# Kernel tuning notes

Measured on AMD Instinct MI355X. Metric: run time of the kernel, lower is better.

Reference implementation:

```python
import jax, jax.numpy as jnp
import numpy as np

N_DRUG, N_TARGET, N_EDGES, H = 50000, 20000, 500000, 256


def setup_inputs() -> dict:
    key = jax.random.key(0)
    ks = jax.random.split(key, 6)
    s = 1.0 / np.sqrt(2 * H)
    return {
        "z_drug": jax.random.normal(ks[0], (N_DRUG, H), dtype=jnp.float32),
        "z_target": jax.random.normal(ks[1], (N_TARGET, H), dtype=jnp.float32),
        "row": jax.random.randint(ks[2], (N_EDGES,), 0, N_DRUG, dtype=jnp.int64),
        "col": jax.random.randint(ks[3], (N_EDGES,), 0, N_TARGET, dtype=jnp.int64),
        "W1": jax.random.normal(ks[4], (2 * H, H), dtype=jnp.float32) * s,
        "b1": jnp.zeros((H,), dtype=jnp.float32),
        "W2": jax.random.normal(ks[5], (H, 1), dtype=jnp.float32) * (1.0 / np.sqrt(H)),
        "b2": jnp.zeros((1,), dtype=jnp.float32),
    }


def reference(z_drug, z_target, row, col, W1, b1, W2, b2):
    # gather endpoint embeddings by edge index, concat -> [E, 2H]
    zc = jnp.concatenate([z_drug[row], z_target[col]], axis=-1)
    h = jax.nn.relu(zc @ W1 + b1)          # [E, H]
    return h @ W2 + b2                     # [E, 1]
```

## Files before the change

kernel.cpp:

```cpp
#include <hip/hip_runtime.h>
#include <hip/hip_bf16.h>
#include <stdint.h>


typedef unsigned short u16;
typedef __attribute__((ext_vector_type(8))) short short8;
typedef __attribute__((ext_vector_type(4))) float f32x4;

#define HDIM 256
#define KDIM 512
#define BM 128
#define BK 64
#define NWAVE 4

__device__ __forceinline__ u16 f2bf(float f) {
  union { float f; uint32_t u; } v; v.f = f;
  uint32_t u = v.u;
  return (u16)((u + 0x7fffu + ((u >> 16) & 1u)) >> 16);
}

__device__ __forceinline__ void gl2lds16(const void* g, void* l) {
  __builtin_amdgcn_global_load_lds(
      (const __attribute__((address_space(1))) unsigned int*)g,
      (__attribute__((address_space(3))) unsigned int*)l,
      16, 0, 0);
}

#define CVT_BLOCKS 4096
__global__ void prep_kernel(const float* __restrict__ zd_f,
                            const float* __restrict__ zt_f,
                            const float* __restrict__ w1,
                            u16* __restrict__ zdb, u16* __restrict__ ztb,
                            u16* __restrict__ w1t, int n4d, int n4t) {
  const int b = blockIdx.x;
  if (b < 32) {
    __shared__ float tile[64][65];
    const int k0 = (b >> 2) * 64, n0 = (b & 3) * 64;
    const int tx = threadIdx.x & 63, ty = threadIdx.x >> 6;
#pragma unroll
    for (int i = ty; i < 64; i += 4)
      tile[i][tx] = w1[(size_t)(k0 + i) * HDIM + n0 + tx];
    __syncthreads();
#pragma unroll
    for (int i = ty; i < 64; i += 4)
      w1t[(size_t)(n0 + i) * KDIM + k0 + tx] = f2bf(tile[tx][i]);
  } else {
    const int idx = (b - 32) * 256 + threadIdx.x;
    const int stride = CVT_BLOCKS * 256;
    for (int i = idx; i < n4d; i += stride) {
      float4 v = ((const float4*)zd_f)[i];
      ushort4 o; o.x = f2bf(v.x); o.y = f2bf(v.y); o.z = f2bf(v.z); o.w = f2bf(v.w);
      ((ushort4*)zdb)[i] = o;
    }
    for (int i = idx; i < n4t; i += stride) {
      float4 v = ((const float4*)zt_f)[i];
      ushort4 o; o.x = f2bf(v.x); o.y = f2bf(v.y); o.z = f2bf(v.z); o.w = f2bf(v.w);
      ((ushort4*)ztb)[i] = o;
    }
  }
}

__global__ __launch_bounds__(256, 2) void edge_mlp_kernel(
    const u16* __restrict__ zd, const u16* __restrict__ zt,
    const int* __restrict__ row, const int* __restrict__ col,
    const u16* __restrict__ w1t, const float* __restrict__ b1,
    const float* __restrict__ w2, const float* __restrict__ b2,
    float* __restrict__ out, int E) {
  __shared__ u16 lA[BM * BK];
  __shared__ u16 lB[HDIM * BK];
  __shared__ float lP[NWAVE * BM];

  const int tid  = threadIdx.x;
  const int wid  = tid >> 6;
  const int lane = tid & 63;
  const int e0   = blockIdx.x * BM;
  const int r8   = lane >> 3;
  const int slog = ((lane & 7) ^ (r8 & 7)) * 8;

  uint32_t offD[4], offT[4];
#pragma unroll
  for (int t = 0; t < 4; ++t) {
    int ge = min(e0 + wid * 32 + r8 + 8 * t, E - 1);
    offD[t] = (uint32_t)row[ge] * HDIM;
    offT[t] = (uint32_t)col[ge] * HDIM;
  }
  const u16* pB = w1t + (uint32_t)(wid * 64 + r8) * KDIM + slog;

  u16* lAw = &lA[(wid * 32) * BK];
  u16* lBw = &lB[(wid * 64) * BK];

  f32x4 acc[8][4];
#pragma unroll
  for (int i = 0; i < 8; ++i)
#pragma unroll
    for (int j = 0; j < 4; ++j) acc[i][j] = f32x4{0.f, 0.f, 0.f, 0.f};

  const int colid = lane & 15;
  const int quad  = lane >> 4;
  const int csw   = colid & 7;

  for (int kc = 0; kc < 8; ++kc) {
    const int koff = (kc & 3) * BK;
    const u16* zbase = (kc < 4) ? zd : zt;

    __syncthreads();
#pragma unroll
    for (int t = 0; t < 4; ++t) {
      uint32_t o = (kc < 4) ? offD[t] : offT[t];
      gl2lds16(zbase + o + koff + slog, lAw + (8 * t) * BK);
    }
#pragma unroll
    for (int j = 0; j < 8; ++j)
      gl2lds16(pB + (size_t)j * 8 * KDIM + kc * BK, lBw + j * 8 * BK);
    __syncthreads();

#pragma unroll
    for (int ks = 0; ks < BK; ks += 32) {
      const int sl = (ks >> 3) + quad;
      short8 aF[8], bF[4];
#pragma unroll
      for (int rt = 0; rt < 8; ++rt)
        aF[rt] = *(const short8*)&lA[(rt * 16 + colid) * BK + ((sl ^ csw) * 8)];
#pragma unroll
      for (int ct = 0; ct < 4; ++ct)
        bF[ct] = *(const short8*)&lB[(wid * 64 + ct * 16 + colid) * BK + ((sl ^ csw) * 8)];
#pragma unroll
      for (int rt = 0; rt < 8; ++rt)
#pragma unroll
        for (int ct = 0; ct < 4; ++ct)
          acc[rt][ct] = __builtin_amdgcn_mfma_f32_16x16x32_bf16(
              aF[rt], bF[ct], acc[rt][ct], 0, 0, 0);
    }
  }

  float b1v[4], w2v[4];
#pragma unroll
  for (int ct = 0; ct < 4; ++ct) {
    int n = wid * 64 + ct * 16 + colid;
    b1v[ct] = b1[n];
    w2v[ct] = w2[n];
  }
#pragma unroll
  for (int rt = 0; rt < 8; ++rt)
#pragma unroll
    for (int j = 0; j < 4; ++j) {
      float s = 0.f;
#pragma unroll
      for (int ct = 0; ct < 4; ++ct)
        s += fmaxf(acc[rt][ct][j] + b1v[ct], 0.f) * w2v[ct];
#pragma unroll
      for (int off = 8; off >= 1; off >>= 1)
        s += __shfl_xor(s, off, 16);
      if (colid == 0)
        lP[wid * BM + rt * 16 + quad * 4 + j] = s;
    }
  __syncthreads();
  if (tid < BM) {
    int ge = e0 + tid;
    if (ge < E)
      out[ge] = lP[tid] + lP[BM + tid] + lP[2 * BM + tid] + lP[3 * BM + tid]
                + b2[0];
  }
}

__global__ void fallback_kernel(
    const float* __restrict__ zd, const float* __restrict__ zt,
    const int* __restrict__ row, const int* __restrict__ col,
    const float* __restrict__ W1, const float* __restrict__ b1,
    const float* __restrict__ W2, const float* __restrict__ b2,
    float* __restrict__ out, int E) {
  __shared__ float zc[16][512];
  __shared__ float red[4][16];
  const int e0 = blockIdx.x * 16;
  const int tid = threadIdx.x;
  for (int i = tid; i < 16 * 512; i += 256) {
    int e = i >> 9, k = i & 511;
    int ge = min(e0 + e, E - 1);
    zc[e][k] = (k < HDIM) ? zd[(size_t)row[ge] * HDIM + k]
                          : zt[(size_t)col[ge] * HDIM + (k - HDIM)];
  }
  __syncthreads();
  float acc[16];
#pragma unroll
  for (int e = 0; e < 16; ++e) acc[e] = 0.f;
  for (int k = 0; k < KDIM; ++k) {
    float w = W1[k * HDIM + tid];
#pragma unroll
    for (int e = 0; e < 16; ++e) acc[e] += zc[e][k] * w;
  }
  float wv = W2[tid], bv = b1[tid];
  const int lane = tid & 63, wid = tid >> 6;
#pragma unroll
  for (int e = 0; e < 16; ++e) {
    float pv = fmaxf(acc[e] + bv, 0.f) * wv;
#pragma unroll
    for (int off = 32; off >= 1; off >>= 1) pv += __shfl_down(pv, off, 64);
    if (lane == 0) red[wid][e] = pv;
  }
  __syncthreads();
  if (tid < 16) {
    int ge = e0 + tid;
    if (ge < E)
      out[ge] = red[0][tid] + red[1][tid] + red[2][tid] + red[3][tid] + b2[0];
  }
}

extern "C" void kernel_launch(void* const* d_in, const int* in_sizes, int n_in,
                              void* d_out, int out_size, void* d_ws, size_t ws_size,
                              hipStream_t stream) {
  const float* zd_f = (const float*)d_in[0];
  const float* zt_f = (const float*)d_in[1];
  const int*   row  = (const int*)d_in[2];
  const int*   col  = (const int*)d_in[3];
  const float* W1   = (const float*)d_in[4];
  const float* b1   = (const float*)d_in[5];
  const float* W2   = (const float*)d_in[6];
  const float* b2   = (const float*)d_in[7];
  float* out = (float*)d_out;

  const int E  = in_sizes[2];
  const int ND = in_sizes[0] / HDIM;
  const int NT = in_sizes[1] / HDIM;

  size_t off_w1t = 0;
  size_t off_zd  = (size_t)KDIM * HDIM * sizeof(u16);
  size_t off_zt  = off_zd + (size_t)ND * HDIM * sizeof(u16);
  size_t need    = off_zt + (size_t)NT * HDIM * sizeof(u16);

  if (ws_size >= need) {
    u16* w1t = (u16*)((char*)d_ws + off_w1t);
    u16* zdb = (u16*)((char*)d_ws + off_zd);
    u16* ztb = (u16*)((char*)d_ws + off_zt);
    int n4d = ND * HDIM / 4, n4t = NT * HDIM / 4;
    prep_kernel<<<32 + CVT_BLOCKS, 256, 0, stream>>>(zd_f, zt_f, W1,
                                                     zdb, ztb, w1t, n4d, n4t);
    edge_mlp_kernel<<<(E + BM - 1) / BM, 256, 0, stream>>>(
        zdb, ztb, row, col, w1t, b1, W2, b2, out, E);
  } else {
    fallback_kernel<<<(E + 15) / 16, 256, 0, stream>>>(
        zd_f, zt_f, row, col, W1, b1, W2, b2, out, E);
  }
}
```

Measured before the change: 280.8 us.

## Double-buffer LDS tiles and enlarge edge block to 256 with 8 waves

The edge MLP kernel now processes 256 edges per block with 512 threads arranged as a 2x4 wave grid. A and B tiles are double-buffered in LDS so the next K-chunk's global-to-LDS loads are issued while MFMAs run on the current chunk, with one barrier per iteration instead of two. The MFMA sequences are wrapped in s_setprio to favour matrix issue. This halves W1 reloads per edge and hides load latency, at the cost of doubling LDS use (about 96KB per block), which may limit occupancy to one block per CU despite the launch bound.

```diff
diff --git a/kernel.cpp b/kernel.cpp
--- a/kernel.cpp
+++ b/kernel.cpp
@@ -9,9 +9,8 @@
 
 #define HDIM 256
 #define KDIM 512
-#define BM 128
+#define BM 256
 #define BK 64
-#define NWAVE 4
 
 __device__ __forceinline__ u16 f2bf(float f) {
   union { float f; uint32_t u; } v; v.f = f;
@@ -60,15 +59,15 @@
   }
 }
 
-__global__ __launch_bounds__(256, 2) void edge_mlp_kernel(
+__global__ __launch_bounds__(512, 2) void edge_mlp_kernel(
     const u16* __restrict__ zd, const u16* __restrict__ zt,
     const int* __restrict__ row, const int* __restrict__ col,
     const u16* __restrict__ w1t, const float* __restrict__ b1,
     const float* __restrict__ w2, const float* __restrict__ b2,
     float* __restrict__ out, int E) {
-  __shared__ u16 lA[BM * BK];
-  __shared__ u16 lB[HDIM * BK];
-  __shared__ float lP[NWAVE * BM];
+  __shared__ u16 lA[2][BM * BK];
+  __shared__ u16 lB[2][HDIM * BK];
+  __shared__ float lP[4 * BM];
 
   const int tid  = threadIdx.x;
   const int wid  = tid >> 6;
@@ -76,6 +75,8 @@
   const int e0   = blockIdx.x * BM;
   const int r8   = lane >> 3;
   const int slog = ((lane & 7) ^ (r8 & 7)) * 8;
+  const int wr   = wid >> 2;
+  const int wc   = wid & 3;
 
   uint32_t offD[4], offT[4];
 #pragma unroll
@@ -84,10 +85,7 @@
     offD[t] = (uint32_t)row[ge] * HDIM;
     offT[t] = (uint32_t)col[ge] * HDIM;
   }
-  const u16* pB = w1t + (uint32_t)(wid * 64 + r8) * KDIM + slog;
-
-  u16* lAw = &lA[(wid * 32) * BK];
-  u16* lBw = &lB[(wid * 64) * BK];
+  const u16* pB = w1t + (uint32_t)(wid * 32 + r8) * KDIM + slog;
 
   f32x4 acc[8][4];
 #pragma unroll
@@ -99,44 +97,57 @@
   const int quad  = lane >> 4;
   const int csw   = colid & 7;
 
-  for (int kc = 0; kc < 8; ++kc) {
+  auto stage = [&](int kc, int buf) {
     const int koff = (kc & 3) * BK;
     const u16* zbase = (kc < 4) ? zd : zt;
-
-    __syncthreads();
+    u16* dA = &lA[buf][(wid * 32) * BK];
+    u16* dB = &lB[buf][(wid * 32) * BK];
 #pragma unroll
     for (int t = 0; t < 4; ++t) {
       uint32_t o = (kc < 4) ? offD[t] : offT[t];
-      gl2lds16(zbase + o + koff + slog, lAw + (8 * t) * BK);
-    }
-#pragma unroll
-    for (int j = 0; j < 8; ++j)
-      gl2lds16(pB + (size_t)j * 8 * KDIM + kc * BK, lBw + j * 8 * BK);
-    __syncthreads();
-
+      gl2lds16(zbase + o + koff + slog, dA + (8 * t) * BK);
+    }
+#pragma unroll
+    for (int j = 0; j < 4; ++j)
+      gl2lds16(pB + (size_t)(j * 8) * KDIM + kc * BK, dB + (j * 8) * BK);
+  };
+
+  stage(0, 0);
+  asm volatile("s_waitcnt vmcnt(0)" ::: "memory");
+  __builtin_amdgcn_s_barrier();
+
+  for (int kc = 0; kc < 8; ++kc) {
+    const int cur = kc & 1;
+    if (kc < 7) stage(kc + 1, cur ^ 1);
+    const u16* A  = lA[cur];
+    const u16* Bm = lB[cur];
 #pragma unroll
     for (int ks = 0; ks < BK; ks += 32) {
       const int sl = (ks >> 3) + quad;
       short8 aF[8], bF[4];
 #pragma unroll
       for (int rt = 0; rt < 8; ++rt)
-        aF[rt] = *(const short8*)&lA[(rt * 16 + colid) * BK + ((sl ^ csw) * 8)];
+        aF[rt] = *(const short8*)&A[(wr * 128 + rt * 16 + colid) * BK + ((sl ^ csw) * 8)];
 #pragma unroll
       for (int ct = 0; ct < 4; ++ct)
-        bF[ct] = *(const short8*)&lB[(wid * 64 + ct * 16 + colid) * BK + ((sl ^ csw) * 8)];
+        bF[ct] = *(const short8*)&Bm[(wc * 64 + ct * 16 + colid) * BK + ((sl ^ csw) * 8)];
+      __builtin_amdgcn_s_setprio(1);
 #pragma unroll
       for (int rt = 0; rt < 8; ++rt)
 #pragma unroll
         for (int ct = 0; ct < 4; ++ct)
           acc[rt][ct] = __builtin_amdgcn_mfma_f32_16x16x32_bf16(
               aF[rt], bF[ct], acc[rt][ct], 0, 0, 0);
-    }
+      __builtin_amdgcn_s_setprio(0);
+    }
+    asm volatile("s_waitcnt vmcnt(0)" ::: "memory");
+    __builtin_amdgcn_s_barrier();
   }
 
   float b1v[4], w2v[4];
 #pragma unroll
   for (int ct = 0; ct < 4; ++ct) {
-    int n = wid * 64 + ct * 16 + colid;
+    int n = wc * 64 + ct * 16 + colid;
     b1v[ct] = b1[n];
     w2v[ct] = w2[n];
   }
@@ -152,7 +163,7 @@
       for (int off = 8; off >= 1; off >>= 1)
         s += __shfl_xor(s, off, 16);
       if (colid == 0)
-        lP[wid * BM + rt * 16 + quad * 4 + j] = s;
+        lP[wc * BM + wr * 128 + rt * 16 + quad * 4 + j] = s;
     }
   __syncthreads();
   if (tid < BM) {
@@ -234,7 +245,7 @@
     int n4d = ND * HDIM / 4, n4t = NT * HDIM / 4;
     prep_kernel<<<32 + CVT_BLOCKS, 256, 0, stream>>>(zd_f, zt_f, W1,
                                                      zdb, ztb, w1t, n4d, n4t);
-    edge_mlp_kernel<<<(E + BM - 1) / BM, 256, 0, stream>>>(
+    edge_mlp_kernel<<<(E + BM - 1) / BM, 512, 0, stream>>>(
         zdb, ztb, row, col, w1t, b1, W2, b2, out, E);
   } else {
     fallback_kernel<<<(E + 15) / 16, 256, 0, stream>>>(
```

New measurement: 291.6 us. 1.04x slower.

## Load gathered A fragments into registers and double-buffer W1 tiles in LDS

Applied to the files above, without the earlier changes.

Each wave now owns 32 edge rows across all 256 hidden columns, loading its gathered z rows directly from global memory into MFMA A-fragment registers instead of staging them through shared memory. W1 tiles are double-buffered in LDS so the next K chunk's loads are issued before the current chunk's MFMAs run, leaving one barrier per chunk. The W2 reduction is done within each wave, removing the cross-wave LDS reduction and its final barrier. In exchange, each wave reads all of B from LDS (four times the previous B traffic), uses 128 accumulator registers, and issues narrower scattered global loads.

```diff
diff --git a/kernel.cpp b/kernel.cpp
--- a/kernel.cpp
+++ b/kernel.cpp
@@ -11,7 +11,6 @@
 #define KDIM 512
 #define BM 128
 #define BK 64
-#define NWAVE 4
 
 __device__ __forceinline__ u16 f2bf(float f) {
   union { float f; uint32_t u; } v; v.f = f;
@@ -66,101 +65,110 @@
     const u16* __restrict__ w1t, const float* __restrict__ b1,
     const float* __restrict__ w2, const float* __restrict__ b2,
     float* __restrict__ out, int E) {
-  __shared__ u16 lA[BM * BK];
-  __shared__ u16 lB[HDIM * BK];
-  __shared__ float lP[NWAVE * BM];
-
-  const int tid  = threadIdx.x;
-  const int wid  = tid >> 6;
-  const int lane = tid & 63;
-  const int e0   = blockIdx.x * BM;
-  const int r8   = lane >> 3;
-  const int slog = ((lane & 7) ^ (r8 & 7)) * 8;
-
-  uint32_t offD[4], offT[4];
-#pragma unroll
-  for (int t = 0; t < 4; ++t) {
-    int ge = min(e0 + wid * 32 + r8 + 8 * t, E - 1);
-    offD[t] = (uint32_t)row[ge] * HDIM;
-    offT[t] = (uint32_t)col[ge] * HDIM;
-  }
-  const u16* pB = w1t + (uint32_t)(wid * 64 + r8) * KDIM + slog;
-
-  u16* lAw = &lA[(wid * 32) * BK];
-  u16* lBw = &lB[(wid * 64) * BK];
-
-  f32x4 acc[8][4];
-#pragma unroll
-  for (int i = 0; i < 8; ++i)
-#pragma unroll
-    for (int j = 0; j < 4; ++j) acc[i][j] = f32x4{0.f, 0.f, 0.f, 0.f};
-
+  __shared__ u16 lB[2][HDIM * BK];
+
+  const int tid   = threadIdx.x;
+  const int wid   = tid >> 6;
+  const int lane  = tid & 63;
+  const int e0    = blockIdx.x * BM;
+  const int r8    = lane >> 3;
+  const int slog  = ((lane & 7) ^ (r8 & 7)) * 8;
   const int colid = lane & 15;
   const int quad  = lane >> 4;
   const int csw   = colid & 7;
 
+  const u16* pB = w1t + (uint32_t)(wid * 64 + r8) * KDIM + slog;
+
+  uint32_t offD2[2], offT2[2];
+#pragma unroll
+  for (int rt = 0; rt < 2; ++rt) {
+    int ge = min(e0 + wid * 32 + rt * 16 + colid, E - 1);
+    offD2[rt] = (uint32_t)row[ge] * HDIM;
+    offT2[rt] = (uint32_t)col[ge] * HDIM;
+  }
+
+  f32x4 acc[2][16];
+#pragma unroll
+  for (int i = 0; i < 2; ++i)
+#pragma unroll
+    for (int j = 0; j < 16; ++j) acc[i][j] = f32x4{0.f, 0.f, 0.f, 0.f};
+
+  short8 aR[2][2][2];
+
+#pragma unroll
+  for (int j = 0; j < 8; ++j)
+    gl2lds16(pB + (size_t)j * 8 * KDIM, &lB[0][(wid * 64 + j * 8) * BK]);
+#pragma unroll
+  for (int rt = 0; rt < 2; ++rt)
+#pragma unroll
+    for (int s = 0; s < 2; ++s)
+      aR[0][rt][s] = *(const short8*)(zd + offD2[rt] + s * 32 + quad * 8);
+  asm volatile("s_waitcnt vmcnt(0)" ::: "memory");
+  __builtin_amdgcn_s_barrier();
+
+#pragma unroll
   for (int kc = 0; kc < 8; ++kc) {
-    const int koff = (kc & 3) * BK;
-    const u16* zbase = (kc < 4) ? zd : zt;
-
-    __syncthreads();
-#pragma unroll
-    for (int t = 0; t < 4; ++t) {
-      uint32_t o = (kc < 4) ? offD[t] : offT[t];
-      gl2lds16(zbase + o + koff + slog, lAw + (8 * t) * BK);
-    }
-#pragma unroll
-    for (int j = 0; j < 8; ++j)
-      gl2lds16(pB + (size_t)j * 8 * KDIM + kc * BK, lBw + j * 8 * BK);
-    __syncthreads();
-
-#pragma unroll
-    for (int ks = 0; ks < BK; ks += 32) {
-      const int sl = (ks >> 3) + quad;
-      short8 aF[8], bF[4];
-#pragma unroll
-      for (int rt = 0; rt < 8; ++rt)
-        aF[rt] = *(const short8*)&lA[(rt * 16 + colid) * BK + ((sl ^ csw) * 8)];
-#pragma unroll
-      for (int ct = 0; ct < 4; ++ct)
-        bF[ct] = *(const short8*)&lB[(wid * 64 + ct * 16 + colid) * BK + ((sl ^ csw) * 8)];
-#pragma unroll
-      for (int rt = 0; rt < 8; ++rt)
-#pragma unroll
-        for (int ct = 0; ct < 4; ++ct)
-          acc[rt][ct] = __builtin_amdgcn_mfma_f32_16x16x32_bf16(
-              aF[rt], bF[ct], acc[rt][ct], 0, 0, 0);
-    }
-  }
-
-  float b1v[4], w2v[4];
-#pragma unroll
-  for (int ct = 0; ct < 4; ++ct) {
-    int n = wid * 64 + ct * 16 + colid;
-    b1v[ct] = b1[n];
-    w2v[ct] = w2[n];
-  }
-#pragma unroll
-  for (int rt = 0; rt < 8; ++rt)
+    const int cur = kc & 1, nxt = cur ^ 1;
+    if (kc < 7) {
+      const int kn = kc + 1;
+      const u16* zb = (kn < 4) ? zd : zt;
+      const uint32_t* offs = (kn < 4) ? offD2 : offT2;
+      const int koffn = (kn & 3) * BK;
+#pragma unroll
+      for (int j = 0; j < 8; ++j)
+        gl2lds16(pB + (size_t)j * 8 * KDIM + kn * BK,
+                 &lB[nxt][(wid * 64 + j * 8) * BK]);
+#pragma unroll
+      for (int rt = 0; rt < 2; ++rt)
+#pragma unroll
+        for (int s = 0; s < 2; ++s)
+          aR[nxt][rt][s] =
+              *(const short8*)(zb + offs[rt] + koffn + s * 32 + quad * 8);
+    }
+#pragma unroll
+    for (int s = 0; s < 2; ++s) {
+      const int sl = s * 4 + quad;
+      __builtin_amdgcn_s_setprio(1);
+#pragma unroll
+      for (int ct = 0; ct < 16; ++ct) {
+        short8 bF = *(const short8*)
+            &lB[cur][(ct * 16 + colid) * BK + ((sl ^ csw) * 8)];
+        acc[0][ct] = __builtin_amdgcn_mfma_f32_16x16x32_bf16(
+            aR[cur][0][s], bF, acc[0][ct], 0, 0, 0);
+        acc[1][ct] = __builtin_amdgcn_mfma_f32_16x16x32_bf16(
+            aR[cur][1][s], bF, acc[1][ct], 0, 0, 0);
+      }
+      __builtin_amdgcn_s_setprio(0);
+    }
+    if (kc < 7) {
+      asm volatile("s_waitcnt vmcnt(0)" ::: "memory");
+      __builtin_amdgcn_s_barrier();
+    }
+  }
+
+  float b1v[16], w2v[16];
+#pragma unroll
+  for (int ct = 0; ct < 16; ++ct) {
+    b1v[ct] = b1[ct * 16 + colid];
+    w2v[ct] = w2[ct * 16 + colid];
+  }
+  const float b2v = b2[0];
+#pragma unroll
+  for (int rt = 0; rt < 2; ++rt)
 #pragma unroll
     for (int j = 0; j < 4; ++j) {
       float s = 0.f;
 #pragma unroll
-      for (int ct = 0; ct < 4; ++ct)
+      for (int ct = 0; ct < 16; ++ct)
         s += fmaxf(acc[rt][ct][j] + b1v[ct], 0.f) * w2v[ct];
 #pragma unroll
       for (int off = 8; off >= 1; off >>= 1)
         s += __shfl_xor(s, off, 16);
-      if (colid == 0)
-        lP[wid * BM + rt * 16 + quad * 4 + j] = s;
-    }
-  __syncthreads();
-  if (tid < BM) {
-    int ge = e0 + tid;
-    if (ge < E)
-      out[ge] = lP[tid] + lP[BM + tid] + lP[2 * BM + tid] + lP[3 * BM + tid]
-                + b2[0];
-  }
+      if (colid == 0) {
+        int ge = e0 + wid * 32 + rt * 16 + quad * 4 + j;
+        if (ge < E) out[ge] = s + b2v;
+      }
+    }
 }
 
 __global__ void fallback_kernel(
```

Result: faster. 265.9 us (-5.3%).
